# Kernel optimization log

Measured on AMD Instinct MI355X. Metric: run time of the kernel, lower is better.

## Reference

```python
import jax, jax.numpy as jnp
import numpy as np

D_MAX = 0.5      # max_dist init kwarg
EPS_W = 1e-8     # weight for far edges
EPS_L = 1e-5     # diagonal jitter on projected Laplacian


def setup_inputs() -> dict:
    key = jax.random.key(0)
    k1, k2, k3, k4, k5 = jax.random.split(key, 5)
    V, d_feat, E, K = 8192, 128, 262144, 512
    # scale so squared distances straddle D_MAX (both branches taken)
    inputs = jax.random.normal(k1, (V, d_feat), dtype=jnp.float32) * 0.05
    src = jax.random.randint(k2, (E,), 0, V)
    off = jax.random.randint(k3, (E,), 1, V)  # avoid self-loops
    dst = (src + off) % V
    edge_index = jnp.stack([src, dst]).astype(jnp.int32)
    A = jax.random.normal(k4, (K, K), dtype=jnp.float32)
    targets = A @ A.T / K + jnp.eye(K, dtype=jnp.float32)  # SPD covariance
    pmat = jax.random.normal(k5, (K, V), dtype=jnp.float32) / np.float32(np.sqrt(V))
    return {"inputs": inputs, "targets": targets, "edge_index": edge_index, "pmat": pmat}


def reference(inputs, targets, edge_index, pmat):
    V = inputs.shape[0]
    K = pmat.shape[0]
    src, dst = edge_index[0], edge_index[1]
    # vectorized per-edge squared distance + thresholded weight
    d = jnp.sum((inputs[src] - inputs[dst]) ** 2, axis=-1)            # [E]
    w = jnp.where(d <= D_MAX, jnp.exp(-d), jnp.float32(EPS_W))        # [E]
    # W = I on diag, w on (i,j) and (j,i) for edges, 0 elsewhere
    W = jnp.eye(V, dtype=inputs.dtype).at[src, dst].set(w).at[dst, src].set(w)
    deg = W.sum(axis=1)                                               # [V]
    idx = jnp.arange(V)
    L = (-W).at[idx, idx].add(deg)                                    # Laplacian D - W
    L_adj = (pmat @ L) @ pmat.T + EPS_L * jnp.eye(K, dtype=inputs.dtype)
    # log det(inv(L_adj)) = -logdet(L_adj); trace(L_adj @ S0) = sum(L_adj * S0^T)
    logdet_Ladj = jnp.linalg.slogdet(L_adj)[1]
    logdet_S0 = jnp.linalg.slogdet(targets)[1]
    tr = jnp.sum(L_adj * targets.T)
    return -logdet_Ladj - logdet_S0 - jnp.float32(K) + tr
```

## Files before the change

### kernel.cpp

```cpp
#include <hip/hip_runtime.h>
#include <math.h>

#define V_N 8192
#define D_F 128
#define E_N 262144
#define K_N 512
#define DMAXF 0.5f
#define EPSW 1e-8f
#define EPSL 1e-5f
#define MAX_SE 16384
#define NZ_SYRK 8

__global__ __launch_bounds__(256) void k_transpose(const float* __restrict__ P, float* __restrict__ PT) {
  __shared__ float tile[32][33];
  int v0 = blockIdx.x * 32, k0 = blockIdx.y * 32;
  int tx = threadIdx.x, ty = threadIdx.y;
#pragma unroll
  for (int i = 0; i < 4; ++i)
    tile[ty + i * 8][tx] = P[(size_t)(k0 + ty + i * 8) * V_N + v0 + tx];
  __syncthreads();
#pragma unroll
  for (int i = 0; i < 4; ++i)
    PT[(size_t)(v0 + ty + i * 8) * K_N + k0 + tx] = tile[tx][ty + i * 8];
}

__global__ __launch_bounds__(256) void k_edge(const float* __restrict__ X, const int* __restrict__ ei,
                                              int* __restrict__ cnt,
                                              int* __restrict__ si, int* __restrict__ sj,
                                              float* __restrict__ sw, unsigned* __restrict__ htab) {
  int t = blockIdx.x * 256 + threadIdx.x;
  int e = t >> 4, lane = t & 15;
  int i = ei[e], j = ei[E_N + e];
  const float4* xi = (const float4*)(X + (size_t)i * D_F);
  const float4* xj = (const float4*)(X + (size_t)j * D_F);
  float4 a0 = xi[lane * 2], a1 = xi[lane * 2 + 1];
  float4 b0 = xj[lane * 2], b1 = xj[lane * 2 + 1];
  float d = 0.f, dx;
  dx = a0.x - b0.x; d += dx * dx;
  dx = a0.y - b0.y; d += dx * dx;
  dx = a0.z - b0.z; d += dx * dx;
  dx = a0.w - b0.w; d += dx * dx;
  dx = a1.x - b1.x; d += dx * dx;
  dx = a1.y - b1.y; d += dx * dx;
  dx = a1.z - b1.z; d += dx * dx;
  dx = a1.w - b1.w; d += dx * dx;
  d += __shfl_xor(d, 1);
  d += __shfl_xor(d, 2);
  d += __shfl_xor(d, 4);
  d += __shfl_xor(d, 8);
  if (lane == 0 && d <= DMAXF) {
    float w = expf(-d);
    unsigned a = (unsigned)min(i, j), b = (unsigned)max(i, j);
    unsigned key = a * 8192u + b;
    unsigned h = (key * 2654435761u) >> 16;
    bool isnew = false;
    for (int probe = 0; probe < 65536; ++probe) {
      unsigned slot = (h + (unsigned)probe) & 65535u;
      unsigned prev = atomicCAS(&htab[slot], 0u, key);
      if (prev == 0u) { isnew = true; break; }
      if (prev == key) break;
    }
    if (isnew) {
      int p = atomicAdd(cnt, 1);
      if (p < MAX_SE) { si[p] = i; sj[p] = j; sw[p] = w; }
    }
  }
}

__global__ __launch_bounds__(256) void k_syrk(const int* __restrict__ cnt, const int* __restrict__ si,
                                              const int* __restrict__ sj, const float* __restrict__ sw,
                                              const float* __restrict__ PT, float* __restrict__ La) {
  int p = blockIdx.x, bj = 0;
  while (p >= 8 - bj) { p -= 8 - bj; ++bj; }
  int bi = bj + p;
  int r0g = bi * 64, c0g = bj * 64;
  int m = min(*cnt, MAX_SE);
  int chunk = (m + NZ_SYRK - 1) / NZ_SYRK;
  int e0 = blockIdx.y * chunk;
  int e1 = min(m, e0 + chunk);

  __shared__ float As[16][68];
  __shared__ float Bs[16][68];
  int tid = threadIdx.x;
  int le = tid >> 4, f = tid & 15;
  int r0 = (tid >> 4) * 4, c0 = (tid & 15) * 4;
  float acc[4][4];
#pragma unroll
  for (int i = 0; i < 4; ++i)
#pragma unroll
    for (int j = 0; j < 4; ++j) acc[i][j] = 0.f;

  for (int es = e0; es < e1; es += 16) {
    int e = es + le;
    float4 qa = make_float4(0.f, 0.f, 0.f, 0.f);
    float4 qb = make_float4(0.f, 0.f, 0.f, 0.f);
    if (e < e1) {
      int i = si[e], j = sj[e];
      float w = sqrtf(sw[e]);
      const float* pi = &PT[(size_t)i * K_N];
      const float* pj = &PT[(size_t)j * K_N];
      float4 ai = *(const float4*)(pi + r0g + f * 4);
      float4 aj = *(const float4*)(pj + r0g + f * 4);
      qa.x = w * (ai.x - aj.x); qa.y = w * (ai.y - aj.y);
      qa.z = w * (ai.z - aj.z); qa.w = w * (ai.w - aj.w);
      if (bi != bj) {
        float4 ci = *(const float4*)(pi + c0g + f * 4);
        float4 cj = *(const float4*)(pj + c0g + f * 4);
        qb.x = w * (ci.x - cj.x); qb.y = w * (ci.y - cj.y);
        qb.z = w * (ci.z - cj.z); qb.w = w * (ci.w - cj.w);
      } else {
        qb = qa;
      }
    }
    __syncthreads();
    *(float4*)&As[le][f * 4] = qa;
    *(float4*)&Bs[le][f * 4] = qb;
    __syncthreads();
#pragma unroll
    for (int k = 0; k < 16; ++k) {
      float4 av = *(const float4*)&As[k][r0];
      float4 bv = *(const float4*)&Bs[k][c0];
      acc[0][0] += av.x * bv.x; acc[0][1] += av.x * bv.y; acc[0][2] += av.x * bv.z; acc[0][3] += av.x * bv.w;
      acc[1][0] += av.y * bv.x; acc[1][1] += av.y * bv.y; acc[1][2] += av.y * bv.z; acc[1][3] += av.y * bv.w;
      acc[2][0] += av.z * bv.x; acc[2][1] += av.z * bv.y; acc[2][2] += av.z * bv.z; acc[2][3] += av.z * bv.w;
      acc[3][0] += av.w * bv.x; acc[3][1] += av.w * bv.y; acc[3][2] += av.w * bv.z; acc[3][3] += av.w * bv.w;
    }
  }
  bool addeps = (blockIdx.y == 0) && (bi == bj);
#pragma unroll
  for (int i = 0; i < 4; ++i)
#pragma unroll
    for (int j = 0; j < 4; ++j) {
      float v = acc[i][j];
      if (addeps && (r0 + i == c0 + j)) v += EPSL;
      atomicAdd(&La[(size_t)(r0g + r0 + i) * K_N + c0g + c0 + j], v);
    }
}

__global__ __launch_bounds__(256) void k_trace(const float* __restrict__ La, const float* __restrict__ T,
                                               float* __restrict__ tr) {
  int idx = blockIdx.x * 256 + threadIdx.x;
  int r = idx >> 9, c = idx & 511;
  float v = 0.f;
  if (r >= c) {
    float scale = (r == c) ? 1.f : 2.f;
    v = scale * La[idx] * T[idx];
  }
  v += __shfl_down(v, 32); v += __shfl_down(v, 16); v += __shfl_down(v, 8);
  v += __shfl_down(v, 4);  v += __shfl_down(v, 2);  v += __shfl_down(v, 1);
  if ((threadIdx.x & 63) == 0) atomicAdd(tr, v);
}

__device__ __forceinline__ void factor32(float (*sm)[65], int o, int tid, float& logacc) {
  if (tid < 64) {
    int r = tid & 31;
    float a[32];
#pragma unroll
    for (int c = 0; c < 32; ++c) a[c] = sm[o + r][o + c];
    float ls = 0.f;
#pragma unroll
    for (int c = 0; c < 32; ++c) {
      float dc = __shfl(a[c], c);
      ls += logf(dc);
      float s_ = sqrtf(dc);
      a[c] = a[c] / s_;
#pragma unroll
      for (int k = c + 1; k < 32; ++k)
        a[k] -= a[c] * __shfl(a[c], k);
    }
    if (tid < 32) {
#pragma unroll
      for (int c = 0; c < 32; ++c) sm[o + r][o + c] = a[c];
    }
    if (tid == 0) logacc += ls;
  }
}

__global__ __launch_bounds__(512) void k_panel(float* La, float* Lw1, float* __restrict__ ld, int s) {
  float* A = (blockIdx.x == 0) ? La : Lw1;
  const int j0 = s * 64;
  int tid = threadIdx.x;
  __shared__ float sm[64][65];
  __shared__ float smT[64][68];
  __shared__ float rinv[64];
  float logacc = 0.f;

  for (int i = tid; i < 4096; i += 512) {
    int r = i >> 6, c = i & 63;
    sm[r][c] = A[(size_t)(j0 + r) * K_N + j0 + c];
  }
  __syncthreads();

  factor32(sm, 0, tid, logacc);
  __syncthreads();

  if (tid < 32) {
    int r = 32 + tid;
    float x[32];
#pragma unroll
    for (int c = 0; c < 32; ++c) x[c] = sm[r][c];
#pragma unroll
    for (int c = 0; c < 32; ++c) {
      x[c] = x[c] / sm[c][c];
#pragma unroll
      for (int k = c + 1; k < 32; ++k)
        x[k] -= x[c] * sm[k][c];
    }
#pragma unroll
    for (int c = 0; c < 32; ++c) sm[r][c] = x[c];
  }
  __syncthreads();

  for (int i = tid; i < 1024; i += 512) {
    int r = 32 + (i >> 5), c = 32 + (i & 31);
    float accv = 0.f;
#pragma unroll
    for (int k = 0; k < 32; ++k) accv += sm[r][k] * sm[c][k];
    sm[r][c] -= accv;
  }
  __syncthreads();

  factor32(sm, 32, tid, logacc);
  __syncthreads();

  for (int i = tid; i < 4096; i += 512) {
    int r = i >> 6, c = i & 63;
    smT[c][r] = sm[r][c];
  }
  if (tid < 64) rinv[tid] = 1.0f / sm[tid][tid];
  __syncthreads();

  int rrow = j0 + 64 + tid;
  if (rrow < K_N) {
    float x[64];
#pragma unroll
    for (int q = 0; q < 16; ++q) {
      float4 f = *(const float4*)&A[(size_t)rrow * K_N + j0 + 4 * q];
      x[4 * q] = f.x; x[4 * q + 1] = f.y; x[4 * q + 2] = f.z; x[4 * q + 3] = f.w;
    }
#pragma unroll
    for (int c = 0; c < 64; ++c) {
      x[c] *= rinv[c];
#pragma unroll
      for (int k = c + 1; k < 64; ++k)
        x[k] -= x[c] * smT[c][k];
    }
#pragma unroll
    for (int q = 0; q < 16; ++q) {
      float4 f;
      f.x = x[4 * q]; f.y = x[4 * q + 1]; f.z = x[4 * q + 2]; f.w = x[4 * q + 3];
      *(float4*)&A[(size_t)rrow * K_N + j0 + 4 * q] = f;
    }
  }

  for (int i = tid; i < 4096; i += 512) {
    int r = i >> 6, c = i & 63;
    A[(size_t)(j0 + r) * K_N + j0 + c] = sm[r][c];
  }
  if (tid == 0) ld[blockIdx.x * 8 + s] = logacc;
}

__global__ __launch_bounds__(256) void k_update(float* La, float* Lw1, int s) {
  float* A = (blockIdx.y == 0) ? La : Lw1;
  int nt = 7 - s;
  int p = blockIdx.x;
  int bj = 0;
  while (p >= nt - bj) { p -= nt - bj; ++bj; }
  int bi = bj + p;
  int r0g = (s + 1 + bi) * 64, c0g = (s + 1 + bj) * 64, k0g = s * 64;

  __shared__ float As[64][68];
  __shared__ float Bs[64][68];
  int tid = threadIdx.x;
  for (int i = tid; i < 1024; i += 256) {
    int r = i >> 4, kq = (i & 15) << 2;
    float4 f = *(const float4*)&A[(size_t)(r0g + r) * K_N + k0g + kq];
    As[kq + 0][r] = f.x; As[kq + 1][r] = f.y; As[kq + 2][r] = f.z; As[kq + 3][r] = f.w;
    float4 g = *(const float4*)&A[(size_t)(c0g + r) * K_N + k0g + kq];
    Bs[kq + 0][r] = g.x; Bs[kq + 1][r] = g.y; Bs[kq + 2][r] = g.z; Bs[kq + 3][r] = g.w;
  }
  __syncthreads();

  int r0 = (tid >> 4) * 4, c0 = (tid & 15) * 4;
  float acc[4][4];
#pragma unroll
  for (int i = 0; i < 4; ++i)
#pragma unroll
    for (int j = 0; j < 4; ++j) acc[i][j] = 0.f;
#pragma unroll 4
  for (int k = 0; k < 64; ++k) {
    float4 av = *(const float4*)&As[k][r0];
    float4 bv = *(const float4*)&Bs[k][c0];
    acc[0][0] += av.x * bv.x; acc[0][1] += av.x * bv.y; acc[0][2] += av.x * bv.z; acc[0][3] += av.x * bv.w;
    acc[1][0] += av.y * bv.x; acc[1][1] += av.y * bv.y; acc[1][2] += av.y * bv.z; acc[1][3] += av.y * bv.w;
    acc[2][0] += av.z * bv.x; acc[2][1] += av.z * bv.y; acc[2][2] += av.z * bv.z; acc[2][3] += av.z * bv.w;
    acc[3][0] += av.w * bv.x; acc[3][1] += av.w * bv.y; acc[3][2] += av.w * bv.z; acc[3][3] += av.w * bv.w;
  }
#pragma unroll
  for (int i = 0; i < 4; ++i) {
    float* cp = &A[(size_t)(r0g + r0 + i) * K_N + c0g + c0];
#pragma unroll
    for (int j = 0; j < 4; ++j) cp[j] = cp[j] - acc[i][j];
  }
}

__global__ void k_combine(const float* __restrict__ ld, const float* __restrict__ tr, float* __restrict__ out) {
  float l0 = 0.f, l1 = 0.f;
#pragma unroll
  for (int s = 0; s < 8; ++s) { l0 += ld[s]; l1 += ld[8 + s]; }
  out[0] = -l0 - l1 - (float)K_N + tr[0];
}

extern "C" void kernel_launch(void* const* d_in, const int* in_sizes, int n_in,
                              void* d_out, int out_size, void* d_ws, size_t ws_size,
                              hipStream_t stream) {
  const float* X  = (const float*)d_in[0];
  const float* T  = (const float*)d_in[1];
  const int*   ei = (const int*)d_in[2];
  const float* P  = (const float*)d_in[3];
  float* out = (float*)d_out;
  char* ws = (char*)d_ws;

  int*      cnt  = (int*)(ws + 0);
  float*    tr   = (float*)(ws + 16);
  float*    ld   = (float*)(ws + 32);
  unsigned* htab = (unsigned*)(ws + 4096);
  float*    La   = (float*)(ws + 266240);
  float*    Lw1  = (float*)(ws + 1314816);
  int*      si   = (int*)(ws + 2363392);
  int*      sj   = (int*)(ws + 2428928);
  float*    sw   = (float*)(ws + 2494464);
  float*    PT   = (float*)(ws + 2560000);

  hipMemsetAsync(ws, 0, 1314816, stream);

  k_transpose<<<dim3(V_N / 32, K_N / 32), dim3(32, 8), 0, stream>>>(P, PT);
  k_edge<<<E_N / 16, 256, 0, stream>>>(X, ei, cnt, si, sj, sw, htab);
  k_syrk<<<dim3(36, NZ_SYRK), 256, 0, stream>>>(cnt, si, sj, sw, PT, La);
  k_trace<<<K_N * K_N / 256, 256, 0, stream>>>(La, T, tr);

  hipMemcpyAsync(Lw1, T, (size_t)K_N * K_N * sizeof(float), hipMemcpyDeviceToDevice, stream);
  for (int s = 0; s < 8; ++s) {
    k_panel<<<2, 512, 0, stream>>>(La, Lw1, ld, s);
    int nt = 7 - s;
    if (nt > 0) k_update<<<dim3(nt * (nt + 1) / 2, 2), 256, 0, stream>>>(La, Lw1, s);
  }
  k_combine<<<1, 1, 0, stream>>>(ld, tr, out);
}
```

Baseline: 637.1 us.

## Fuse pre-pass kernels, fold trace into SYRK, prefetch SYRK edges, raise split count

Merges the P transpose, edge-weight/hash dedup pass and the T→Lw1 copy into one heterogeneous launch, which removes two launches and a memcpy. The trace reduction moves into the SYRK epilogue, using each block's partial accumulators, so the separate k_trace pass over La disappears. The SYRK loop now register-prefetches the next 16 edges' PT rows while the current tile is being computed, and the edge split rises from 8 to 24 for more blocks. The cost is more atomics on La and on the trace scalar, and a more complex branchy pre-kernel.

Result: faster. 553.0 us (-13.2%).

```diff
diff --git a/kernel.cpp b/kernel.cpp
--- a/kernel.cpp
+++ b/kernel.cpp
@@ -9,67 +9,78 @@
 #define EPSW 1e-8f
 #define EPSL 1e-5f
 #define MAX_SE 16384
-#define NZ_SYRK 8
-
-__global__ __launch_bounds__(256) void k_transpose(const float* __restrict__ P, float* __restrict__ PT) {
+#define NZ_SYRK 24
+
+#define NB_TR 4096
+#define NB_ED (E_N / 16)
+#define NB_CP 256
+
+__global__ __launch_bounds__(256) void k_pre(const float* __restrict__ P, float* __restrict__ PT,
+                                             const float* __restrict__ X, const int* __restrict__ ei,
+                                             int* __restrict__ cnt, int* __restrict__ si,
+                                             int* __restrict__ sj, float* __restrict__ sw,
+                                             unsigned* __restrict__ htab,
+                                             const float* __restrict__ T, float* __restrict__ Lw1) {
   __shared__ float tile[32][33];
-  int v0 = blockIdx.x * 32, k0 = blockIdx.y * 32;
-  int tx = threadIdx.x, ty = threadIdx.y;
-#pragma unroll
-  for (int i = 0; i < 4; ++i)
-    tile[ty + i * 8][tx] = P[(size_t)(k0 + ty + i * 8) * V_N + v0 + tx];
-  __syncthreads();
-#pragma unroll
-  for (int i = 0; i < 4; ++i)
-    PT[(size_t)(v0 + ty + i * 8) * K_N + k0 + tx] = tile[tx][ty + i * 8];
-}
-
-__global__ __launch_bounds__(256) void k_edge(const float* __restrict__ X, const int* __restrict__ ei,
-                                              int* __restrict__ cnt,
-                                              int* __restrict__ si, int* __restrict__ sj,
-                                              float* __restrict__ sw, unsigned* __restrict__ htab) {
-  int t = blockIdx.x * 256 + threadIdx.x;
-  int e = t >> 4, lane = t & 15;
-  int i = ei[e], j = ei[E_N + e];
-  const float4* xi = (const float4*)(X + (size_t)i * D_F);
-  const float4* xj = (const float4*)(X + (size_t)j * D_F);
-  float4 a0 = xi[lane * 2], a1 = xi[lane * 2 + 1];
-  float4 b0 = xj[lane * 2], b1 = xj[lane * 2 + 1];
-  float d = 0.f, dx;
-  dx = a0.x - b0.x; d += dx * dx;
-  dx = a0.y - b0.y; d += dx * dx;
-  dx = a0.z - b0.z; d += dx * dx;
-  dx = a0.w - b0.w; d += dx * dx;
-  dx = a1.x - b1.x; d += dx * dx;
-  dx = a1.y - b1.y; d += dx * dx;
-  dx = a1.z - b1.z; d += dx * dx;
-  dx = a1.w - b1.w; d += dx * dx;
-  d += __shfl_xor(d, 1);
-  d += __shfl_xor(d, 2);
-  d += __shfl_xor(d, 4);
-  d += __shfl_xor(d, 8);
-  if (lane == 0 && d <= DMAXF) {
-    float w = expf(-d);
-    unsigned a = (unsigned)min(i, j), b = (unsigned)max(i, j);
-    unsigned key = a * 8192u + b;
-    unsigned h = (key * 2654435761u) >> 16;
-    bool isnew = false;
-    for (int probe = 0; probe < 65536; ++probe) {
-      unsigned slot = (h + (unsigned)probe) & 65535u;
-      unsigned prev = atomicCAS(&htab[slot], 0u, key);
-      if (prev == 0u) { isnew = true; break; }
-      if (prev == key) break;
-    }
-    if (isnew) {
-      int p = atomicAdd(cnt, 1);
-      if (p < MAX_SE) { si[p] = i; sj[p] = j; sw[p] = w; }
-    }
+  int b = blockIdx.x;
+  if (b < NB_TR) {
+    int v0 = (b & 255) * 32, k0 = (b >> 8) * 32;
+    int tx = threadIdx.x & 31, ty = threadIdx.x >> 5;
+#pragma unroll
+    for (int i = 0; i < 4; ++i)
+      tile[ty + i * 8][tx] = P[(size_t)(k0 + ty + i * 8) * V_N + v0 + tx];
+    __syncthreads();
+#pragma unroll
+    for (int i = 0; i < 4; ++i)
+      PT[(size_t)(v0 + ty + i * 8) * K_N + k0 + tx] = tile[tx][ty + i * 8];
+  } else if (b < NB_TR + NB_ED) {
+    int t = (b - NB_TR) * 256 + threadIdx.x;
+    int e = t >> 4, lane = t & 15;
+    int i = ei[e], j = ei[E_N + e];
+    const float4* xi = (const float4*)(X + (size_t)i * D_F);
+    const float4* xj = (const float4*)(X + (size_t)j * D_F);
+    float4 a0 = xi[lane * 2], a1 = xi[lane * 2 + 1];
+    float4 b0 = xj[lane * 2], b1 = xj[lane * 2 + 1];
+    float d = 0.f, dx;
+    dx = a0.x - b0.x; d += dx * dx;
+    dx = a0.y - b0.y; d += dx * dx;
+    dx = a0.z - b0.z; d += dx * dx;
+    dx = a0.w - b0.w; d += dx * dx;
+    dx = a1.x - b1.x; d += dx * dx;
+    dx = a1.y - b1.y; d += dx * dx;
+    dx = a1.z - b1.z; d += dx * dx;
+    dx = a1.w - b1.w; d += dx * dx;
+    d += __shfl_xor(d, 1);
+    d += __shfl_xor(d, 2);
+    d += __shfl_xor(d, 4);
+    d += __shfl_xor(d, 8);
+    if (lane == 0 && d <= DMAXF) {
+      float w = expf(-d);
+      unsigned a = (unsigned)min(i, j), bb = (unsigned)max(i, j);
+      unsigned key = a * 8192u + bb;
+      unsigned h = (key * 2654435761u) >> 16;
+      bool isnew = false;
+      for (int probe = 0; probe < 65536; ++probe) {
+        unsigned slot = (h + (unsigned)probe) & 65535u;
+        unsigned prev = atomicCAS(&htab[slot], 0u, key);
+        if (prev == 0u) { isnew = true; break; }
+        if (prev == key) break;
+      }
+      if (isnew) {
+        int p = atomicAdd(cnt, 1);
+        if (p < MAX_SE) { si[p] = i; sj[p] = j; sw[p] = w; }
+      }
+    }
+  } else {
+    int idx = (b - NB_TR - NB_ED) * 256 + threadIdx.x;
+    ((float4*)Lw1)[idx] = ((const float4*)T)[idx];
   }
 }
 
 __global__ __launch_bounds__(256) void k_syrk(const int* __restrict__ cnt, const int* __restrict__ si,
                                               const int* __restrict__ sj, const float* __restrict__ sw,
-                                              const float* __restrict__ PT, float* __restrict__ La) {
+                                              const float* __restrict__ PT, float* __restrict__ La,
+                                              const float* __restrict__ T, float* __restrict__ tr) {
   int p = blockIdx.x, bj = 0;
   while (p >= 8 - bj) { p -= 8 - bj; ++bj; }
   int bi = bj + p;
@@ -90,32 +101,57 @@
 #pragma unroll
     for (int j = 0; j < 4; ++j) acc[i][j] = 0.f;
 
-  for (int es = e0; es < e1; es += 16) {
-    int e = es + le;
-    float4 qa = make_float4(0.f, 0.f, 0.f, 0.f);
-    float4 qb = make_float4(0.f, 0.f, 0.f, 0.f);
+  float w_ = 0.f;
+  float4 ai = make_float4(0.f, 0.f, 0.f, 0.f), aj = ai, ci = ai, cj = ai;
+  {
+    int e = e0 + le;
     if (e < e1) {
       int i = si[e], j = sj[e];
-      float w = sqrtf(sw[e]);
+      w_ = sw[e];
       const float* pi = &PT[(size_t)i * K_N];
       const float* pj = &PT[(size_t)j * K_N];
-      float4 ai = *(const float4*)(pi + r0g + f * 4);
-      float4 aj = *(const float4*)(pj + r0g + f * 4);
-      qa.x = w * (ai.x - aj.x); qa.y = w * (ai.y - aj.y);
-      qa.z = w * (ai.z - aj.z); qa.w = w * (ai.w - aj.w);
+      ai = *(const float4*)(pi + r0g + f * 4);
+      aj = *(const float4*)(pj + r0g + f * 4);
       if (bi != bj) {
-        float4 ci = *(const float4*)(pi + c0g + f * 4);
-        float4 cj = *(const float4*)(pj + c0g + f * 4);
-        qb.x = w * (ci.x - cj.x); qb.y = w * (ci.y - cj.y);
-        qb.z = w * (ci.z - cj.z); qb.w = w * (ci.w - cj.w);
-      } else {
-        qb = qa;
+        ci = *(const float4*)(pi + c0g + f * 4);
+        cj = *(const float4*)(pj + c0g + f * 4);
       }
+    }
+  }
+
+  for (int es = e0; es < e1; es += 16) {
+    float sq = sqrtf(w_);
+    float4 qa, qb;
+    qa.x = sq * (ai.x - aj.x); qa.y = sq * (ai.y - aj.y);
+    qa.z = sq * (ai.z - aj.z); qa.w = sq * (ai.w - aj.w);
+    if (bi != bj) {
+      qb.x = sq * (ci.x - cj.x); qb.y = sq * (ci.y - cj.y);
+      qb.z = sq * (ci.z - cj.z); qb.w = sq * (ci.w - cj.w);
+    } else {
+      qb = qa;
     }
     __syncthreads();
     *(float4*)&As[le][f * 4] = qa;
     *(float4*)&Bs[le][f * 4] = qb;
     __syncthreads();
+
+    {
+      int e = es + 16 + le;
+      w_ = 0.f;
+      if (e < e1) {
+        int i = si[e], j = sj[e];
+        w_ = sw[e];
+        const float* pi = &PT[(size_t)i * K_N];
+        const float* pj = &PT[(size_t)j * K_N];
+        ai = *(const float4*)(pi + r0g + f * 4);
+        aj = *(const float4*)(pj + r0g + f * 4);
+        if (bi != bj) {
+          ci = *(const float4*)(pi + c0g + f * 4);
+          cj = *(const float4*)(pj + c0g + f * 4);
+        }
+      }
+    }
+
 #pragma unroll
     for (int k = 0; k < 16; ++k) {
       float4 av = *(const float4*)&As[k][r0];
@@ -126,29 +162,23 @@
       acc[3][0] += av.w * bv.x; acc[3][1] += av.w * bv.y; acc[3][2] += av.w * bv.z; acc[3][3] += av.w * bv.w;
     }
   }
+
   bool addeps = (blockIdx.y == 0) && (bi == bj);
+  float tdot = 0.f;
 #pragma unroll
   for (int i = 0; i < 4; ++i)
 #pragma unroll
     for (int j = 0; j < 4; ++j) {
       float v = acc[i][j];
-      if (addeps && (r0 + i == c0 + j)) v += EPSL;
-      atomicAdd(&La[(size_t)(r0g + r0 + i) * K_N + c0g + c0 + j], v);
-    }
-}
-
-__global__ __launch_bounds__(256) void k_trace(const float* __restrict__ La, const float* __restrict__ T,
-                                               float* __restrict__ tr) {
-  int idx = blockIdx.x * 256 + threadIdx.x;
-  int r = idx >> 9, c = idx & 511;
-  float v = 0.f;
-  if (r >= c) {
-    float scale = (r == c) ? 1.f : 2.f;
-    v = scale * La[idx] * T[idx];
-  }
-  v += __shfl_down(v, 32); v += __shfl_down(v, 16); v += __shfl_down(v, 8);
-  v += __shfl_down(v, 4);  v += __shfl_down(v, 2);  v += __shfl_down(v, 1);
-  if ((threadIdx.x & 63) == 0) atomicAdd(tr, v);
+      int rg = r0g + r0 + i, cg = c0g + c0 + j;
+      if (addeps && rg == cg) v += EPSL;
+      atomicAdd(&La[(size_t)rg * K_N + cg], v);
+      float sc = (bi != bj) ? 2.f : (rg == cg ? 1.f : (rg > cg ? 2.f : 0.f));
+      if (sc != 0.f) tdot += sc * v * T[(size_t)rg * K_N + cg];
+    }
+  tdot += __shfl_down(tdot, 32); tdot += __shfl_down(tdot, 16); tdot += __shfl_down(tdot, 8);
+  tdot += __shfl_down(tdot, 4);  tdot += __shfl_down(tdot, 2);  tdot += __shfl_down(tdot, 1);
+  if ((tid & 63) == 0) atomicAdd(tr, tdot);
 }
 
 __device__ __forceinline__ void factor32(float (*sm)[65], int o, int tid, float& logacc) {
@@ -334,12 +364,9 @@
 
   hipMemsetAsync(ws, 0, 1314816, stream);
 
-  k_transpose<<<dim3(V_N / 32, K_N / 32), dim3(32, 8), 0, stream>>>(P, PT);
-  k_edge<<<E_N / 16, 256, 0, stream>>>(X, ei, cnt, si, sj, sw, htab);
-  k_syrk<<<dim3(36, NZ_SYRK), 256, 0, stream>>>(cnt, si, sj, sw, PT, La);
-  k_trace<<<K_N * K_N / 256, 256, 0, stream>>>(La, T, tr);
-
-  hipMemcpyAsync(Lw1, T, (size_t)K_N * K_N * sizeof(float), hipMemcpyDeviceToDevice, stream);
+  k_pre<<<NB_TR + NB_ED + NB_CP, 256, 0, stream>>>(P, PT, X, ei, cnt, si, sj, sw, htab, T, Lw1);
+  k_syrk<<<dim3(36, NZ_SYRK), 256, 0, stream>>>(cnt, si, sj, sw, PT, La, T, tr);
+
   for (int s = 0; s < 8; ++s) {
     k_panel<<<2, 512, 0, stream>>>(La, Lw1, ld, s);
     int nt = 7 - s;
```
